# Performance work log

Measured on AMD Instinct MI355X. Metric: run time of the kernel, lower is better.

Reference implementation:

```python
import jax, jax.numpy as jnp
import numpy as np

B, H, L, D, S = 32, 1, 4096, 64, 512  # batch, heads(=1, codebook shared), seq, d_k, n_code
PE_LAM = 100000.0
EPS = 1e-6


def _sinusoid_embs(length, width, lam):
    # standard sinusoid table [length, width]: concat(sin, cos)
    pos = jnp.arange(length, dtype=jnp.float32)
    inv_lams = lam ** (-jnp.arange(0, width, 2, dtype=jnp.float32) / width)
    pre = pos[:, None] * inv_lams[None, :]
    return jnp.concatenate([jnp.sin(pre), jnp.cos(pre)], axis=-1)


def _codebook():
    # get_codebook: sinusoids -> rms-norm (center/gain/bias off) -> tau^{-1/2} scale -> stop-grad -> [1,S,D]
    c = _sinusoid_embs(S, D, PE_LAM)
    c = c * jax.lax.rsqrt(jnp.mean(jnp.square(c), axis=-1, keepdims=True) + EPS)
    tau = float(D) ** 0.5
    return jax.lax.stop_gradient((tau ** -0.5) * c)[None, ...]  # [H=1, S, D]


def setup_inputs() -> dict:
    key = jax.random.key(0)
    vecs = jax.random.normal(key, (B, H, L, D), dtype=jnp.float32)
    loss_mask = jnp.ones((B, L), dtype=jnp.float32)
    return {"vecs": vecs, "loss_mask": loss_mask}


def reference(vecs, loss_mask):
    c = _codebook()  # [1, S, D]
    # pairwise squared distances [B,H,L,S] via ||v||^2 - 2 v.c + ||c||^2
    diffs2 = (
        jnp.sum(jnp.square(vecs), axis=-1)[..., None]
        - 2.0 * jnp.einsum("bhlk,hsk->bhls", vecs, c)
        + jnp.sum(jnp.square(c), axis=-1)[None, :, None, :]
    )
    z = jnp.argmin(diffs2, axis=-1).astype(jnp.int32)       # [B,H,L]
    errs2 = jax.nn.relu(jnp.min(diffs2, axis=-1))           # [B,H,L]
    # gather codewords: codebook [1,1,S,D], indices [B,H,L,1]
    cz = jnp.take_along_axis(c[None, ...], z[..., None], axis=2)  # [B,H,L,D]
    # straight-through estimator
    quantized = jax.lax.stop_gradient(cz) + vecs - jax.lax.stop_gradient(vecs)
    # l_commit = mean over (B,L) of sum over heads of masked errs2
    l_commit = jnp.mean(jnp.sum(loss_mask[:, None, :] * errs2, axis=1))
    return quantized, z, l_commit, errs2
```

## Files before the change

kernel.cpp:

```cpp
#include <hip/hip_runtime.h>
#include <math.h>

#define NB 32
#define NL 4096
#define ND 64
#define NS 512
#define NTOK (NB*NL)

#define OFF_Q 0
#define OFF_Z (NTOK*ND)
#define OFF_LC (OFF_Z + NTOK)
#define OFF_E (OFF_LC + 1)

typedef __attribute__((ext_vector_type(8))) short short8;
typedef __attribute__((ext_vector_type(4))) float f32x4;
typedef unsigned int u32;
typedef unsigned short u16;
typedef unsigned long long u64;

#define QCODES 128
#define TOKS 256
#define TPB 1024
#define SLOTS 32
#define EPS_H 1e-3f
#define NBLK (NTOK / TOKS)

__device__ __forceinline__ u32 f2bf_rne(float x) {
    u32 u = __float_as_uint(x);
    return (u + 0x7fffu + ((u >> 16) & 1u)) >> 16;
}

__device__ __forceinline__ void upd_key(u64& best, float dist, int code) {
    u32 u = __float_as_uint(dist);
    u ^= (u >> 31) ? 0xFFFFFFFFu : 0x80000000u;
    u64 k = ((u64)u << 32) | (u32)code;
    if (k < best) best = k;
}

__global__ void cb_kernel(float* __restrict__ cb, float* __restrict__ cc,
                          u16* __restrict__ cbh, u16* __restrict__ cbl) {
    int s = blockIdx.x;
    int d = threadIdx.x;
    int j = (d < 32) ? d : (d - 32);
    double e = -(double)(2 * j) / 64.0;
    double invlam = pow(100000.0, e);
    double pre = (double)s * invlam;
    float val = (float)((d < 32) ? sin(pre) : cos(pre));

    float sq = val * val;
    #pragma unroll
    for (int off = 32; off > 0; off >>= 1) sq += __shfl_xor(sq, off);
    float mean = sq * (1.0f / 64.0f);
    float scale = (1.0f / sqrtf(mean + 1e-6f)) * 0.35355339059327379f;
    float c = val * scale;
    cb[s * ND + d] = c;

    float c2 = c * c;
    #pragma unroll
    for (int off = 32; off > 0; off >>= 1) c2 += __shfl_xor(c2, off);
    if (d == 0) cc[s] = c2;

    u32 hb = f2bf_rne(c);
    float hf = __uint_as_float(hb << 16);
    u32 lb = f2bf_rne(c - hf);
    int g = d >> 3, ee = d & 7;
    int pos = s * 64 + (((g ^ (s & 7)) << 3) | ee);
    cbh[pos] = (u16)hb;
    cbl[pos] = (u16)lb;
}

__launch_bounds__(TPB)
__global__ void fused_kernel(const float* __restrict__ vecs,
                             const float* __restrict__ mask,
                             const float* __restrict__ cb,
                             const float* __restrict__ cc,
                             const u16* __restrict__ cbh,
                             const u16* __restrict__ cbl,
                             float* __restrict__ outq,
                             float* __restrict__ outz,
                             float* __restrict__ oute,
                             float* __restrict__ partial) {
    __shared__ float4 svec[TOKS * 16];
    __shared__ u16 ldsH[QCODES * 64];
    __shared__ u16 ldsL[QCODES * 64];
    __shared__ u16 slots[TOKS][SLOTS];
    __shared__ float hval[TOKS][SLOTS];
    __shared__ u32 cnt_l[TOKS];
    __shared__ int z_l[TOKS];
    __shared__ float wsum[TPB / 64];

    const int tid = threadIdx.x;
    const int grp = blockIdx.x;
    const int w = tid >> 6;
    const int lane = tid & 63;
    const int c16 = lane & 15;
    const int h = lane >> 4;

    {
        const float4* vsrc = (const float4*)(vecs + (size_t)grp * TOKS * ND);
        #pragma unroll
        for (int i = 0; i < 4; ++i) {
            int idx = i * TPB + tid;
            int row = idx >> 4, g = idx & 15;
            svec[row * 16 + (g ^ (row & 15))] = vsrc[idx];
        }
        if (tid < TOKS) cnt_l[tid] = 0;
    }
    ((short8*)ldsH)[tid] = ((const short8*)cbh)[tid];
    ((short8*)ldsL)[tid] = ((const short8*)cbl)[tid];
    __syncthreads();

    const int trow = w * 16 + c16;
    short8 bh[2], bl[2];
    #pragma unroll
    for (int kk = 0; kk < 2; ++kk) {
        float x[8];
        #pragma unroll
        for (int u = 0; u < 2; ++u) {
            int g = kk * 8 + h * 2 + u;
            float4 t = svec[trow * 16 + (g ^ (trow & 15))];
            x[u * 4 + 0] = t.x; x[u * 4 + 1] = t.y;
            x[u * 4 + 2] = t.z; x[u * 4 + 3] = t.w;
        }
        short8 H, L;
        #pragma unroll
        for (int e2 = 0; e2 < 8; ++e2) {
            u32 hb = f2bf_rne(x[e2]);
            float hf = __uint_as_float(hb << 16);
            u32 lb = f2bf_rne(x[e2] - hf);
            H[e2] = (short)hb; L[e2] = (short)lb;
        }
        bh[kk] = H; bl[kk] = L;
    }

    for (int q = 0; q < 4; ++q) {
        if (q) {
            __syncthreads();
            ((short8*)ldsH)[tid] = ((const short8*)(cbh + q * QCODES * 64))[tid];
            ((short8*)ldsL)[tid] = ((const short8*)(cbl + q * QCODES * 64))[tid];
            __syncthreads();
        }
        #pragma unroll
        for (int c = 0; c < 2; ++c) {
            f32x4 acc[4];
            #pragma unroll
            for (int mt = 0; mt < 4; ++mt) {
                int cr = q * QCODES + c * 64 + mt * 16 + h * 4;
                f32x4 ini;
                ini[0] = -0.5f * cc[cr + 0];
                ini[1] = -0.5f * cc[cr + 1];
                ini[2] = -0.5f * cc[cr + 2];
                ini[3] = -0.5f * cc[cr + 3];
                acc[mt] = ini;
            }
            #pragma unroll
            for (int mt = 0; mt < 4; ++mt) {
                int code_l = c * 64 + mt * 16 + c16;
                int sw = code_l & 7;
                short8 ah[2], al[2];
                #pragma unroll
                for (int kk = 0; kk < 2; ++kk) {
                    int off = code_l * 64 + (((kk * 4 + h) ^ sw) << 3);
                    ah[kk] = *(const short8*)(ldsH + off);
                    al[kk] = *(const short8*)(ldsL + off);
                }
                #pragma unroll
                for (int kk = 0; kk < 2; ++kk) {
                    acc[mt] = __builtin_amdgcn_mfma_f32_16x16x32_bf16(ah[kk], bh[kk], acc[mt], 0, 0, 0);
                    acc[mt] = __builtin_amdgcn_mfma_f32_16x16x32_bf16(ah[kk], bl[kk], acc[mt], 0, 0, 0);
                    acc[mt] = __builtin_amdgcn_mfma_f32_16x16x32_bf16(al[kk], bh[kk], acc[mt], 0, 0, 0);
                }
            }
            float m = acc[0][0];
            #pragma unroll
            for (int mt = 0; mt < 4; ++mt) {
                m = fmaxf(m, fmaxf(fmaxf(acc[mt][0], acc[mt][1]),
                                   fmaxf(acc[mt][2], acc[mt][3])));
            }
            m = fmaxf(m, __shfl_xor(m, 16));
            m = fmaxf(m, __shfl_xor(m, 32));
            float thr = m - EPS_H;
            #pragma unroll
            for (int mt = 0; mt < 4; ++mt) {
                #pragma unroll
                for (int r = 0; r < 4; ++r) {
                    float v = acc[mt][r];
                    if (v >= thr) {
                        u32 pos = atomicAdd(&cnt_l[trow], 1u);
                        if (pos < (u32)SLOTS) {
                            slots[trow][pos] = (u16)(q * QCODES + c * 64 + mt * 16 + h * 4 + r);
                            hval[trow][pos] = v;
                        }
                    }
                }
            }
        }
    }
    __syncthreads();

    const int p  = tid >> 2;
    const int qs = tid & 3;
    const int tok = grp * TOKS + p;

    float4 vf[16];
    #pragma unroll
    for (int g = 0; g < 16; ++g) vf[g] = svec[p * 16 + (g ^ (p & 15))];
    float vv;
    {
        float a0 = 0.f, a1 = 0.f, a2 = 0.f, a3 = 0.f;
        #pragma unroll
        for (int i = 0; i < 16; ++i) {
            a0 = fmaf(vf[i].x, vf[i].x, a0);
            a1 = fmaf(vf[i].y, vf[i].y, a1);
            a2 = fmaf(vf[i].z, vf[i].z, a2);
            a3 = fmaf(vf[i].w, vf[i].w, a3);
        }
        vv = (a0 + a1) + (a2 + a3);
    }

    u32 cnt = cnt_l[p]; if (cnt > (u32)SLOTS) cnt = (u32)SLOTS;
    float hm = -3.4e38f;
    for (u32 j2 = 0; j2 < cnt; ++j2) hm = fmaxf(hm, hval[p][j2]);
    float thr2 = hm - EPS_H;

    u64 best = 0xFFFFFFFFFFFFFFFFull;
    for (u32 j2 = qs; j2 < cnt; j2 += 4) {
        if (hval[p][j2] >= thr2) {
            int code = (int)slots[p][j2];
            const float4* cs = (const float4*)(cb + (size_t)code * ND);
            float d0 = 0.f, d1 = 0.f, d2 = 0.f, d3 = 0.f;
            #pragma unroll
            for (int i2 = 0; i2 < 16; ++i2) {
                float4 cv = cs[i2];
                d0 = fmaf(cv.x, vf[i2].x, d0);
                d1 = fmaf(cv.y, vf[i2].y, d1);
                d2 = fmaf(cv.z, vf[i2].z, d2);
                d3 = fmaf(cv.w, vf[i2].w, d3);
            }
            float dot = (d0 + d1) + (d2 + d3);
            float dist = (vv - 2.0f * dot) + cc[code];
            upd_key(best, dist, code);
        }
    }
    {
        u64 o = __shfl_xor(best, 1); if (o < best) best = o;
        o = __shfl_xor(best, 2); if (o < best) best = o;
    }

    float contrib = 0.0f;
    if (qs == 0) {
        int zi = (int)(best & 0xFFFFFFFFu);
        u32 du = (u32)(best >> 32);
        du ^= (du >> 31) ? 0x80000000u : 0xFFFFFFFFu;
        float dmin = __uint_as_float(du);
        float err = fmaxf(dmin, 0.0f);
        outz[tok] = (float)zi;
        oute[tok] = err;
        z_l[p] = zi;
        contrib = mask[tok] * err;
    }
    #pragma unroll
    for (int off = 32; off > 0; off >>= 1) contrib += __shfl_xor(contrib, off);
    if (lane == 0) wsum[w] = contrib;
    __syncthreads();
    if (tid == 0) {
        float t = 0.f;
        #pragma unroll
        for (int i = 0; i < TPB / 64; ++i) t += wsum[i];
        partial[grp] = t;
    }

    const float4* cb4 = (const float4*)cb;
    float4* qo = (float4*)(outq + (size_t)grp * TOKS * ND);
    #pragma unroll
    for (int i = 0; i < 4; ++i) {
        int gidx = i * TPB + tid;
        int t2 = gidx >> 4;
        int sub = gidx & 15;
        qo[gidx] = cb4[(size_t)z_l[t2] * 16 + sub];
    }
}

__global__ void fin_kernel(const float* __restrict__ partial, float* __restrict__ outl) {
    int t = threadIdx.x;
    float x = partial[t];
    #pragma unroll
    for (int off = 32; off > 0; off >>= 1) x += __shfl_xor(x, off);
    __shared__ float ws[8];
    if ((t & 63) == 0) ws[t >> 6] = x;
    __syncthreads();
    if (t == 0) {
        float s = 0.f;
        #pragma unroll
        for (int i = 0; i < 8; ++i) s += ws[i];
        outl[0] = s / (float)NTOK;
    }
}

extern "C" void kernel_launch(void* const* d_in, const int* in_sizes, int n_in,
                              void* d_out, int out_size, void* d_ws, size_t ws_size,
                              hipStream_t stream) {
    const float* vecs = (const float*)d_in[0];
    const float* mask = (const float*)d_in[1];

    float* out = (float*)d_out;
    float* outq = out + OFF_Q;
    float* outz = out + OFF_Z;
    float* outl = out + OFF_LC;
    float* oute = out + OFF_E;

    float* ws_f = (float*)d_ws;
    float* cb = ws_f;
    float* cc = ws_f + 32768;
    u16*  cbh = (u16*)(ws_f + 33280);
    u16*  cbl = (u16*)(ws_f + 49664);
    float* partial = ws_f + 66048;

    cb_kernel<<<NS, 64, 0, stream>>>(cb, cc, cbh, cbl);
    fused_kernel<<<NBLK, TPB, 0, stream>>>(vecs, mask, cb, cc, cbh, cbl,
                                           outq, outz, oute, partial);
    fin_kernel<<<1, 512, 0, stream>>>(partial, outl);
}
```

Baseline: 75.94 us.

## Halve block size, shrink candidate slot buffers, and pad slot rows

```diff
diff --git a/kernel.cpp b/kernel.cpp
--- a/kernel.cpp
+++ b/kernel.cpp
@@ -19,9 +19,10 @@
 typedef unsigned long long u64;
 
 #define QCODES 128
-#define TOKS 256
-#define TPB 1024
-#define SLOTS 32
+#define TOKS 128
+#define TPB 512
+#define SLOTS 12
+#define SLOTP 13
 #define EPS_H 1e-3f
 #define NBLK (NTOK / TOKS)
 
@@ -69,7 +70,7 @@
     cbl[pos] = (u16)lb;
 }
 
-__launch_bounds__(TPB)
+__launch_bounds__(TPB, 4)
 __global__ void fused_kernel(const float* __restrict__ vecs,
                              const float* __restrict__ mask,
                              const float* __restrict__ cb,
@@ -83,8 +84,8 @@
     __shared__ float4 svec[TOKS * 16];
     __shared__ u16 ldsH[QCODES * 64];
     __shared__ u16 ldsL[QCODES * 64];
-    __shared__ u16 slots[TOKS][SLOTS];
-    __shared__ float hval[TOKS][SLOTS];
+    __shared__ u32 slots[TOKS * SLOTP];
+    __shared__ float hval[TOKS * SLOTP];
     __shared__ u32 cnt_l[TOKS];
     __shared__ int z_l[TOKS];
     __shared__ float wsum[TPB / 64];
@@ -106,8 +107,12 @@
         }
         if (tid < TOKS) cnt_l[tid] = 0;
     }
-    ((short8*)ldsH)[tid] = ((const short8*)cbh)[tid];
-    ((short8*)ldsL)[tid] = ((const short8*)cbl)[tid];
+    #pragma unroll
+    for (int i = 0; i < 2; ++i) {
+        int k = i * TPB + tid;
+        ((short8*)ldsH)[k] = ((const short8*)cbh)[k];
+        ((short8*)ldsL)[k] = ((const short8*)cbl)[k];
+    }
     __syncthreads();
 
     const int trow = w * 16 + c16;
@@ -136,8 +141,12 @@
     for (int q = 0; q < 4; ++q) {
         if (q) {
             __syncthreads();
-            ((short8*)ldsH)[tid] = ((const short8*)(cbh + q * QCODES * 64))[tid];
-            ((short8*)ldsL)[tid] = ((const short8*)(cbl + q * QCODES * 64))[tid];
+            #pragma unroll
+            for (int i = 0; i < 2; ++i) {
+                int k = i * TPB + tid;
+                ((short8*)ldsH)[k] = ((const short8*)(cbh + q * QCODES * 64))[k];
+                ((short8*)ldsL)[k] = ((const short8*)(cbl + q * QCODES * 64))[k];
+            }
             __syncthreads();
         }
         #pragma unroll
@@ -188,8 +197,8 @@
                     if (v >= thr) {
                         u32 pos = atomicAdd(&cnt_l[trow], 1u);
                         if (pos < (u32)SLOTS) {
-                            slots[trow][pos] = (u16)(q * QCODES + c * 64 + mt * 16 + h * 4 + r);
-                            hval[trow][pos] = v;
+                            slots[trow * SLOTP + pos] = (u32)(q * QCODES + c * 64 + mt * 16 + h * 4 + r);
+                            hval[trow * SLOTP + pos] = v;
                         }
                     }
                 }
@@ -220,13 +229,13 @@
 
     u32 cnt = cnt_l[p]; if (cnt > (u32)SLOTS) cnt = (u32)SLOTS;
     float hm = -3.4e38f;
-    for (u32 j2 = 0; j2 < cnt; ++j2) hm = fmaxf(hm, hval[p][j2]);
+    for (u32 j2 = 0; j2 < cnt; ++j2) hm = fmaxf(hm, hval[p * SLOTP + j2]);
     float thr2 = hm - EPS_H;
 
     u64 best = 0xFFFFFFFFFFFFFFFFull;
     for (u32 j2 = qs; j2 < cnt; j2 += 4) {
-        if (hval[p][j2] >= thr2) {
-            int code = (int)slots[p][j2];
+        if (hval[p * SLOTP + j2] >= thr2) {
+            int code = (int)slots[p * SLOTP + j2];
             const float4* cs = (const float4*)(cb + (size_t)code * ND);
             float d0 = 0.f, d1 = 0.f, d2 = 0.f, d3 = 0.f;
             #pragma unroll
@@ -286,13 +295,13 @@
     float x = partial[t];
     #pragma unroll
     for (int off = 32; off > 0; off >>= 1) x += __shfl_xor(x, off);
-    __shared__ float ws[8];
+    __shared__ float ws[16];
     if ((t & 63) == 0) ws[t >> 6] = x;
     __syncthreads();
     if (t == 0) {
         float s = 0.f;
         #pragma unroll
-        for (int i = 0; i < 8; ++i) s += ws[i];
+        for (int i = 0; i < 16; ++i) s += ws[i];
         outl[0] = s / (float)NTOK;
     }
 }
@@ -319,5 +328,5 @@
     cb_kernel<<<NS, 64, 0, stream>>>(cb, cc, cbh, cbl);
     fused_kernel<<<NBLK, TPB, 0, stream>>>(vecs, mask, cb, cc, cbh, cbl,
                                            outq, outz, oute, partial);
-    fin_kernel<<<1, 512, 0, stream>>>(partial, outl);
-}
+    fin_kernel<<<1, 1024, 0, stream>>>(partial, outl);
+}
```

After: 68.52 us, median of 2. -9.8%, faster.
